# Kernel optimization log

Hardware: AMD Instinct MI355X
Metric: run time of the kernel (lower is better)

Reference implementation:

```python
import jax, jax.numpy as jnp
import numpy as np
from jax import lax

# Fixed dims from MSSMamba defaults
B_, L_, DM = 2, 8192, 256
NH, HP, NS = 4, 64, 8          # nheads, headdim, d_state
DIN = NH * HP                  # d_inner = 256
DPROJ = 2 * DIN + 2 * NS + NH  # 532


def setup_inputs() -> dict:
    key = jax.random.key(0)
    ks = jax.random.split(key, 16)
    f = lambda k, s, sc=1.0: jax.random.normal(k, s, jnp.float32) * sc
    inp = {
        'x_H': f(ks[0], (B_, L_, DM)),
        'x_V': f(ks[1], (B_, L_, DM)),
        'W_in_H': f(ks[2], (DM, 2 * DPROJ), 0.05),
        'W_in_V': f(ks[3], (DM, 2 * DPROJ), 0.05),
        'W_out_HF': f(ks[4], (DIN, DM), 0.05),
        'W_out_HB': f(ks[5], (DIN, DM), 0.05),
        'W_out_VF': f(ks[6], (DIN, DM), 0.05),
        'W_out_VB': f(ks[7], (DIN, DM), 0.05),
        'W_out': f(ks[8], (4 * DM, DM), 0.05),
    }
    for i, nm in enumerate(['HF', 'HB', 'VF', 'VB']):
        kd = jax.random.fold_in(ks[9], i)
        ka = jax.random.fold_in(ks[10], i)
        inp['dt_bias_' + nm] = f(kd, (NH,), 0.1)
        inp['A_log_' + nm] = jnp.log(jax.random.uniform(ka, (NH,), jnp.float32, 1.0, 16.0))
        inp['D_' + nm] = jnp.ones((NH,), jnp.float32)
    # per-batch permutation mapping vertical position -> horizontal position
    inp['v2h'] = jax.vmap(lambda k: jax.random.permutation(k, L_))(
        jax.random.split(ks[11], B_)).astype(jnp.int32)
    return inp


def _scan_dir(zxbcdt, dt_bias, A_log, D):
    # zxbcdt: [b, l, DPROJ] -> Mamba2-style selective scan, ngroups=1
    z = zxbcdt[..., :DIN].reshape(B_, L_, NH, HP)
    xBC = jax.nn.silu(zxbcdt[..., DIN:DIN + DIN + 2 * NS])
    x = xBC[..., :DIN].reshape(B_, L_, NH, HP)
    Bm = xBC[..., DIN:DIN + NS]      # [b, l, n]
    Cm = xBC[..., DIN + NS:]         # [b, l, n]
    dt = jax.nn.softplus(zxbcdt[..., -NH:] + dt_bias)  # [b, l, h]
    A = -jnp.exp(A_log)              # [h]
    dA = jnp.exp(dt * A)             # [b, l, h]
    dBx = jnp.einsum('blh,bln,blhp->blhpn', dt, Bm, x)  # [b,l,h,p,n]

    def step(state, inp):
        dA_t, dBx_t, C_t = inp
        state = dA_t[..., None, None] * state + dBx_t   # [b,h,p,n]
        y_t = jnp.einsum('bhpn,bn->bhp', state, C_t)
        return state, y_t

    init = jnp.zeros((B_, NH, HP, NS), dt.dtype)
    _, ys = lax.scan(step, init, (jnp.moveaxis(dA, 1, 0),
                                  jnp.moveaxis(dBx, 1, 0),
                                  jnp.moveaxis(Cm, 1, 0)))
    y = jnp.moveaxis(ys, 0, 1) + D[None, None, :, None] * x  # skip D*x
    y = y * jax.nn.silu(z)                                   # gate
    return y.reshape(B_, L_, DIN)


def reference(x_H, x_V, W_in_H, W_in_V,
              dt_bias_HF, dt_bias_HB, dt_bias_VF, dt_bias_VB,
              A_log_HF, A_log_HB, A_log_VF, A_log_VB,
              D_HF, D_HB, D_VF, D_VB,
              W_out_HF, W_out_HB, W_out_VF, W_out_VB,
              W_out, v2h):
    zx_HF, zx_HB = jnp.split(x_H @ W_in_H, 2, axis=-1)
    zx_VF, zx_VB = jnp.split(x_V @ W_in_V, 2, axis=-1)
    # note: source applies out_proj_HB to the HF branch (kept faithful)
    y_HF = _scan_dir(zx_HF, dt_bias_HF, A_log_HF, D_HF) @ W_out_HB
    y_HB = _scan_dir(zx_HB[:, ::-1], dt_bias_HB, A_log_HB, D_HB)[:, ::-1] @ W_out_HF
    y_VF = _scan_dir(zx_VF, dt_bias_VF, A_log_VF, D_VF) @ W_out_VB
    y_VB = _scan_dir(zx_VB[:, ::-1], dt_bias_VB, A_log_VB, D_VB)[:, ::-1] @ W_out_VF
    # remap vertical-ordered outputs to horizontal ordering (scatter by v2h)
    bidx = jnp.arange(B_)[:, None]
    y_VF = jnp.zeros_like(y_VF).at[bidx, v2h].set(y_VF)
    y_VB = jnp.zeros_like(y_VB).at[bidx, v2h].set(y_VB)
    cat = jnp.concatenate([y_HF, y_HB, y_VF, y_VB], axis=-1)  # [b, l, 4*d_model]
    return jax.nn.silu(cat) @ W_out
```

## Files before the change

### kernel.cpp

```cpp
#include <hip/hip_runtime.h>
#include <hip/hip_bf16.h>

#define B_N 2
#define L_N 8192
#define ROWS 16384
#define CHUNK 32
#define NCHUNK 256
#define NPAD 1152

typedef __bf16 bf16x8 __attribute__((ext_vector_type(8)));
typedef float f32x4 __attribute__((ext_vector_type(4)));

__device__ __forceinline__ float siluf(float v) {
  return v * __builtin_amdgcn_rcpf(1.f + __expf(-v));
}
__device__ __forceinline__ float softplusf_(float v) {
  return fmaxf(v, 0.f) + log1pf(__expf(-fabsf(v)));
}
__device__ __forceinline__ unsigned short f2bf(float v) {
  union { __bf16 b; unsigned short u; } x;
  x.b = (__bf16)v;
  return x.u;
}
__device__ __forceinline__ float bf2f(unsigned short u) {
  union { unsigned u; float f; } x; x.u = ((unsigned)u) << 16;
  return x.f;
}

__device__ __forceinline__ void gload_lds16(const unsigned short* g, unsigned short* l) {
  __builtin_amdgcn_global_load_lds(
      (const __attribute__((address_space(1))) unsigned int*)g,
      (__attribute__((address_space(3))) unsigned int*)l, 16, 0, 0);
}

struct P4 { const float* p[4]; };
struct ScanConsts {
  const float* dt_bias[4];
  const float* A_log[4];
  const float* D[4];
};

__global__ __launch_bounds__(256) void k_prep(
    const float* __restrict__ xH, const float* __restrict__ xV,
    const float* __restrict__ WH, const float* __restrict__ WV,
    P4 ws, const float* __restrict__ W_out, ScanConsts sc,
    unsigned short* __restrict__ xbf, float* __restrict__ dtv_arr, float* __restrict__ dA_arr,
    unsigned short* __restrict__ Wt_in, unsigned short* __restrict__ Wt_dirs,
    unsigned short* __restrict__ Wt_fin) {
  __shared__ float xs[32][257];
  __shared__ float Wsm[8][260];
  int bid = blockIdx.x;
  int tid = threadIdx.x;
  if (bid < 1024) {
    const int mat = bid >> 9;
    const float* x = mat ? xV : xH;
    const float* W = mat ? WV : WH;
    const int r0 = (bid & 511) * 32;
    for (int i = tid; i < 2048; i += 256) {
      int c = i >> 8, k = i & 255;
      int sl = c >> 2, h = c & 3;
      Wsm[c][k] = W[(long)k * 1064 + sl * 532 + 528 + h];
    }
    for (int i = tid; i < 32 * 64; i += 256) {
      int rl = i >> 6, kq = (i & 63) * 4;
      float4 v = *(const float4*)(x + (long)(r0 + rl) * 256 + kq);
      xs[rl][kq + 0] = v.x; xs[rl][kq + 1] = v.y; xs[rl][kq + 2] = v.z; xs[rl][kq + 3] = v.w;
    }
    __syncthreads();
    for (int i = tid; i < 32 * 64; i += 256) {
      int rl = i >> 6, kq = (i & 63) * 4;
      ushort4 o;
      o.x = f2bf(xs[rl][kq + 0]);
      o.y = f2bf(xs[rl][kq + 1]);
      o.z = f2bf(xs[rl][kq + 2]);
      o.w = f2bf(xs[rl][kq + 3]);
      *(ushort4*)(xbf + (size_t)mat * ROWS * 256 + (long)(r0 + rl) * 256 + kq) = o;
    }
    const int rl = tid >> 3, c = tid & 7;
    float s = 0.f;
    #pragma unroll 8
    for (int k = 0; k < 256; ++k) s = fmaf(xs[rl][k], Wsm[c][k], s);
    const int sl = c >> 2, h = c & 3;
    const int dir = mat * 2 + sl;
    float dtv = softplusf_(s + sc.dt_bias[dir][h]);
    float dAv = __expf(dtv * (-__expf(sc.A_log[dir][h])));
    long o = ((long)dir * 4 + h) * ROWS + (r0 + rl);
    dtv_arr[o] = dtv;
    dA_arr[o] = dAv;
  } else if (bid < 3328) {
    int i = (bid - 1024) * 256 + tid;
    int z = i / (NPAD * 256);
    int rem = i - z * (NPAD * 256);
    int n = rem >> 8, k = rem & 255;
    const float* W = z ? WV : WH;
    int sl = n >= 544;
    int cc = n - (sl ? 544 : 0);
    float v = (cc < 532) ? W[(long)k * 1064 + sl * 532 + cc] : 0.f;
    Wt_in[i] = f2bf(v);
  } else if (bid < 4352) {
    int i = (bid - 3328) * 256 + tid;
    int d = i >> 16;
    int rem = i & 65535;
    int n = rem >> 8, k = rem & 255;
    Wt_dirs[i] = f2bf(ws.p[d][(long)k * 256 + n]);
  } else {
    int i = (bid - 4352) * 256 + tid;
    int n = i >> 10, k = i & 1023;
    Wt_fin[i] = f2bf(W_out[(long)k * 256 + n]);
  }
}

struct EpiIn {
  unsigned short* zraw;
  unsigned short* xraw;
  unsigned short* bc;
};

__global__ __launch_bounds__(256) void k_gemm_in(
    const unsigned short* __restrict__ Abase, const unsigned short* __restrict__ Btbase,
    EpiIn ep) {
  __shared__ unsigned short As[128 * 32];
  __shared__ unsigned short Bs[128 * 32];
  __shared__ unsigned short trs[4][16 * 72];
  const int tid = threadIdx.x;
  const int lane = tid & 63;
  const int wid = tid >> 6;
  const int wm = wid & 1, wn = wid >> 1;
  const int q = lane >> 4, r = lane & 15;
  const int m0 = blockIdx.x * 128;
  const int n0 = blockIdx.y * 128;
  const int z = blockIdx.z;
  const unsigned short* A = Abase + (long)z * ROWS * 256;
  const unsigned short* Bt = Btbase + (long)z * NPAD * 256;

  f32x4 acc[4][4] = {};
  const int swr = (r >> 1) & 3;

  for (int kt = 0; kt < 256; kt += 32) {
    #pragma unroll
    for (int i = 0; i < 2; ++i) {
      int idx = i * 256 + tid;
      int row = idx >> 2;
      int ch = (idx & 3) ^ ((row >> 1) & 3);
      gload_lds16(A + (long)(m0 + row) * 256 + kt + ch * 8,
                  &As[(size_t)(i * 256 + wid * 64) * 8]);
    }
    #pragma unroll
    for (int i = 0; i < 2; ++i) {
      int idx = i * 256 + tid;
      int row = idx >> 2;
      int ch = (idx & 3) ^ ((row >> 1) & 3);
      gload_lds16(Bt + (long)(n0 + row) * 256 + kt + ch * 8,
                  &Bs[(size_t)(i * 256 + wid * 64) * 8]);
    }
    __syncthreads();
    bf16x8 af[4], bfr[4];
    #pragma unroll
    for (int mi = 0; mi < 4; ++mi)
      af[mi] = *(const bf16x8*)&As[((wm * 64 + mi * 16 + r) * 4 + (q ^ swr)) * 8];
    #pragma unroll
    for (int ni = 0; ni < 4; ++ni)
      bfr[ni] = *(const bf16x8*)&Bs[((wn * 64 + ni * 16 + r) * 4 + (q ^ swr)) * 8];
    #pragma unroll
    for (int mi = 0; mi < 4; ++mi)
      #pragma unroll
      for (int ni = 0; ni < 4; ++ni)
        acc[mi][ni] = __builtin_amdgcn_mfma_f32_16x16x32_bf16(af[mi], bfr[ni], acc[mi][ni], 0, 0, 0);
    __syncthreads();
  }

  unsigned short* tr = trs[wid];
  #pragma unroll
  for (int mi = 0; mi < 4; ++mi) {
    #pragma unroll
    for (int ni = 0; ni < 4; ++ni)
      #pragma unroll
      for (int j = 0; j < 4; ++j)
        tr[(q * 4 + j) * 72 + ni * 16 + r] = f2bf(acc[mi][ni][j]);
    asm volatile("s_waitcnt lgkmcnt(0)" ::: "memory");
    #pragma unroll
    for (int pass = 0; pass < 2; ++pass) {
      int rl = pass * 8 + (lane >> 3);
      int c8 = (lane & 7) * 8;
      bf16x8 v = *(const bf16x8*)&tr[rl * 72 + c8];
      int row = m0 + wm * 64 + mi * 16 + rl;
      int col = n0 + wn * 64 + c8;
      int sl = col >= 544;
      int cc = col - (sl ? 544 : 0);
      if (cc < 528) {
        int dir = z * 2 + sl;
        if (cc < 256)
          *(bf16x8*)(ep.zraw + ((long)dir * ROWS + row) * 256 + cc) = v;
        else if (cc < 512)
          *(bf16x8*)(ep.xraw + ((long)dir * ROWS + row) * 256 + cc - 256) = v;
        else
          *(bf16x8*)(ep.bc + ((long)dir * ROWS + row) * 16 + cc - 512) = v;
      }
    }
    asm volatile("s_waitcnt lgkmcnt(0)" ::: "memory");
  }
}

__global__ __launch_bounds__(512, 4) void k_fuse(
    const unsigned short* __restrict__ ybf,
    const unsigned short* __restrict__ Wt_dirs,
    const unsigned short* __restrict__ Wt_fin,
    unsigned short* __restrict__ pbuf) {
  __shared__ unsigned short Ab[2][64 * 32];
  __shared__ unsigned short Bb[2][256 * 32];
  __shared__ unsigned short Tl[64 * 264];
  const int tid = threadIdx.x;
  const int lane = tid & 63;
  const int wid = tid >> 6;
  const int wm = wid & 1, wn = wid >> 1;
  const int q = lane >> 4, r = lane & 15;
  const int r0 = blockIdx.x * 64;
  const int pair = blockIdx.y;
  const int swr = (r >> 1) & 3;

  const int a_row = tid >> 2;
  const int a_ch = (tid & 3) ^ ((a_row >> 1) & 3);
  const long a_off = (long)(r0 + a_row) * 256 + a_ch * 8;
  int b_row[2], b_ch[2];
  #pragma unroll
  for (int rnd = 0; rnd < 2; ++rnd) {
    int idx = rnd * 512 + tid;
    b_row[rnd] = idx >> 2;
    b_ch[rnd] = (idx & 3) ^ ((b_row[rnd] >> 1) & 3);
  }

  f32x4 acc_o[2][4] = {};
  int cur = 0;

  {
    const unsigned short* yd = ybf + (long)(pair * 2) * ROWS * 256;
    const unsigned short* Wd = Wt_dirs + (long)(pair * 2) * 65536;
    if (tid < 256)
      gload_lds16(yd + a_off, &Ab[0][(size_t)(wid * 64) * 8]);
    #pragma unroll
    for (int rnd = 0; rnd < 2; ++rnd)
      gload_lds16(Wd + (long)b_row[rnd] * 256 + b_ch[rnd] * 8,
                  &Bb[0][(size_t)(rnd * 512 + wid * 64) * 8]);
  }
  __syncthreads();

  #pragma unroll
  for (int dd = 0; dd < 2; ++dd) {
    const int d = pair * 2 + dd;
    const unsigned short* yd = ybf + (long)d * ROWS * 256;
    const unsigned short* Wd = Wt_dirs + (long)d * 65536;

    f32x4 acc_t[2][4] = {};
    for (int kt8 = 0; kt8 < 8; ++kt8) {
      const int kt = kt8 * 32;
      if (kt8 < 7) {
        if (tid < 256)
          gload_lds16(yd + a_off + kt + 32, &Ab[cur ^ 1][(size_t)(wid * 64) * 8]);
        #pragma unroll
        for (int rnd = 0; rnd < 2; ++rnd)
          gload_lds16(Wd + (long)b_row[rnd] * 256 + kt + 32 + b_ch[rnd] * 8,
                      &Bb[cur ^ 1][(size_t)(rnd * 512 + wid * 64) * 8]);
      } else {
        #pragma unroll
        for (int rnd = 0; rnd < 2; ++rnd)
          gload_lds16(Wt_fin + (long)b_row[rnd] * 1024 + d * 256 + b_ch[rnd] * 8,
                      &Bb[cur ^ 1][(size_t)(rnd * 512 + wid * 64) * 8]);
      }
      bf16x8 af[2], bfr[4];
      #pragma unroll
      for (int mi = 0; mi < 2; ++mi)
        af[mi] = *(const bf16x8*)&Ab[cur][((wm * 32 + mi * 16 + r) * 4 + (q ^ swr)) * 8];
      #pragma unroll
      for (int ni = 0; ni < 4; ++ni)
        bfr[ni] = *(const bf16x8*)&Bb[cur][((wn * 64 + ni * 16 + r) * 4 + (q ^ swr)) * 8];
      __builtin_amdgcn_s_setprio(1);
      #pragma unroll
      for (int mi = 0; mi < 2; ++mi)
        #pragma unroll
        for (int ni = 0; ni < 4; ++ni)
          acc_t[mi][ni] = __builtin_amdgcn_mfma_f32_16x16x32_bf16(af[mi], bfr[ni], acc_t[mi][ni], 0, 0, 0);
      __builtin_amdgcn_s_setprio(0);
      __syncthreads();
      cur ^= 1;
    }
    #pragma unroll
    for (int mi = 0; mi < 2; ++mi)
      #pragma unroll
      for (int ni = 0; ni < 4; ++ni)
        #pragma unroll
        for (int j = 0; j < 4; ++j)
          Tl[(wm * 32 + mi * 16 + q * 4 + j) * 264 + wn * 64 + ni * 16 + r] =
              f2bf(siluf(acc_t[mi][ni][j]));
    __syncthreads();
    for (int kt8 = 0; kt8 < 8; ++kt8) {
      const int kt = kt8 * 32;
      if (kt8 < 7) {
        #pragma unroll
        for (int rnd = 0; rnd < 2; ++rnd)
          gload_lds16(Wt_fin + (long)b_row[rnd] * 1024 + d * 256 + kt + 32 + b_ch[rnd] * 8,
                      &Bb[cur ^ 1][(size_t)(rnd * 512 + wid * 64) * 8]);
      } else if (dd == 0) {
        const unsigned short* yd1 = ybf + (long)(d + 1) * ROWS * 256;
        const unsigned short* Wd1 = Wt_dirs + (long)(d + 1) * 65536;
        if (tid < 256)
          gload_lds16(yd1 + a_off, &Ab[cur ^ 1][(size_t)(wid * 64) * 8]);
        #pragma unroll
        for (int rnd = 0; rnd < 2; ++rnd)
          gload_lds16(Wd1 + (long)b_row[rnd] * 256 + b_ch[rnd] * 8,
                      &Bb[cur ^ 1][(size_t)(rnd * 512 + wid * 64) * 8]);
      }
      bf16x8 af[2], bfr[4];
      #pragma unroll
      for (int mi = 0; mi < 2; ++mi)
        af[mi] = *(const bf16x8*)&Tl[(wm * 32 + mi * 16 + r) * 264 + kt + q * 8];
      #pragma unroll
      for (int ni = 0; ni < 4; ++ni)
        bfr[ni] = *(const bf16x8*)&Bb[cur][((wn * 64 + ni * 16 + r) * 4 + (q ^ swr)) * 8];
      __builtin_amdgcn_s_setprio(1);
      #pragma unroll
      for (int mi = 0; mi < 2; ++mi)
        #pragma unroll
        for (int ni = 0; ni < 4; ++ni)
          acc_o[mi][ni] = __builtin_amdgcn_mfma_f32_16x16x32_bf16(af[mi], bfr[ni], acc_o[mi][ni], 0, 0, 0);
      __builtin_amdgcn_s_setprio(0);
      __syncthreads();
      cur ^= 1;
    }
  }

  #pragma unroll
  for (int mi = 0; mi < 2; ++mi)
    #pragma unroll
    for (int ni = 0; ni < 4; ++ni)
      #pragma unroll
      for (int j = 0; j < 4; ++j)
        Tl[(wm * 32 + mi * 16 + q * 4 + j) * 264 + wn * 64 + ni * 16 + r] = f2bf(acc_o[mi][ni][j]);
  __syncthreads();
  unsigned short* pout = pbuf + (long)pair * ROWS * 256;
  #pragma unroll
  for (int pass = 0; pass < 4; ++pass) {
    int id = pass * 512 + tid;
    int row = id >> 5, c8 = (id & 31) * 8;
    bf16x8 v = *(const bf16x8*)&Tl[row * 264 + c8];
    *(bf16x8*)(pout + (long)(r0 + row) * 256 + c8) = v;
  }
}

__global__ void k_red(const unsigned short* __restrict__ pbuf, float* __restrict__ out) {
  int i = blockIdx.x * 256 + threadIdx.x;
  uint4 a = ((const uint4*)pbuf)[i];
  uint4 b = ((const uint4*)(pbuf + (size_t)ROWS * 256))[i];
  const unsigned short* au = (const unsigned short*)&a;
  const unsigned short* bu = (const unsigned short*)&b;
  float rr[8];
  #pragma unroll
  for (int j = 0; j < 8; ++j) rr[j] = bf2f(au[j]) + bf2f(bu[j]);
  ((float4*)out)[i * 2] = *(float4*)&rr[0];
  ((float4*)out)[i * 2 + 1] = *(float4*)&rr[4];
}

struct ScanP {
  const unsigned short* xraw;
  const unsigned short* zraw;
  const unsigned short* bc;
  const float* dtv;
  const float* dA;
  const float* D[4];
};

__global__ __launch_bounds__(64) void k_scan1(ScanP sp, float* __restrict__ S,
                                              float* __restrict__ P) {
  __shared__ __align__(16) float Bst[CHUNK][8];
  __shared__ float dAs[CHUNK];
  const int p = threadIdx.x;
  const int c = blockIdx.x;
  const int bh = blockIdx.y;
  const int d = blockIdx.z;
  const int b = bh >> 2, h = bh & 3;
  const int rev = d & 1;
  const int t0 = c * CHUNK;
  if (p < CHUNK) {
    const int t = t0 + p;
    const int l = rev ? (L_N - 1 - t) : t;
    const int row = (b << 13) + l;
    uint4 bv = *(const uint4*)(sp.bc + ((long)d * ROWS + row) * 16);
    const unsigned short* bu = (const unsigned short*)&bv;
    float dtvv = sp.dtv[((long)d * 4 + h) * ROWS + row];
    dAs[p] = sp.dA[((long)d * 4 + h) * ROWS + row];
    #pragma unroll
    for (int n = 0; n < 8; ++n) Bst[p][n] = siluf(bf2f(bu[n])) * dtvv;
  }
  __syncthreads();

  float st[8] = {0, 0, 0, 0, 0, 0, 0, 0};
  float cumdA = 1.f;
  const int l0 = rev ? (L_N - 1 - t0) : t0;
  const unsigned short* xp = sp.xraw + ((long)d * ROWS + (b << 13) + l0) * 256 + h * 64 + p;
  const long stp = rev ? -256L : 256L;

  unsigned short xa[8], xb[8];
  #pragma unroll
  for (int j = 0; j < 8; ++j) xa[j] = xp[(long)j * stp];
  #pragma unroll
  for (int g = 0; g < 4; ++g) {
    if (g < 3) {
      #pragma unroll
      for (int j = 0; j < 8; ++j) xb[j] = xp[(long)((g + 1) * 8 + j) * stp];
    }
    #pragma unroll
    for (int j = 0; j < 8; ++j) {
      int s = g * 8 + j;
      float x = siluf(bf2f(xa[j]));
      float dA = dAs[s];
      f32x4 B0 = *(const f32x4*)&Bst[s][0];
      f32x4 B1 = *(const f32x4*)&Bst[s][4];
      cumdA *= dA;
      st[0] = fmaf(dA, st[0], x * B0[0]);
      st[1] = fmaf(dA, st[1], x * B0[1]);
      st[2] = fmaf(dA, st[2], x * B0[2]);
      st[3] = fmaf(dA, st[3], x * B0[3]);
      st[4] = fmaf(dA, st[4], x * B1[0]);
      st[5] = fmaf(dA, st[5], x * B1[1]);
      st[6] = fmaf(dA, st[6], x * B1[2]);
      st[7] = fmaf(dA, st[7], x * B1[3]);
    }
    #pragma unroll
    for (int j = 0; j < 8; ++j) xa[j] = xb[j];
  }
  float* Sp = S + ((((long)d * NCHUNK + c) * 8 + bh) * 64 + p) * 8;
  #pragma unroll
  for (int n = 0; n < 8; ++n) Sp[n] = st[n];
  if (p == 0) P[((long)d * NCHUNK + c) * 8 + bh] = cumdA;
}

__global__ __launch_bounds__(512) void k_scan2(const float* __restrict__ S,
                                               const float* __restrict__ P,
                                               float* __restrict__ carry) {
  __shared__ float Pl[NCHUNK];
  const int tid = threadIdx.x;
  const int dbh = blockIdx.x;
  const int d = dbh >> 3, bh = dbh & 7;
  if (tid < NCHUNK) Pl[tid] = P[((long)d * NCHUNK + tid) * 8 + bh];
  __syncthreads();
  float cy = 0.f;
  carry[(((long)d * NCHUNK + 0) * 8 + bh) * 512 + tid] = 0.f;
  #pragma unroll 8
  for (int c = 1; c < NCHUNK; ++c) {
    const float Sv = S[(((long)d * NCHUNK + (c - 1)) * 8 + bh) * 512 + tid];
    cy = fmaf(Pl[c - 1], cy, Sv);
    carry[(((long)d * NCHUNK + c) * 8 + bh) * 512 + tid] = cy;
  }
}

__global__ __launch_bounds__(64) void k_scan3(ScanP sp, const float* __restrict__ carry,
                                              const int* __restrict__ v2h,
                                              unsigned short* __restrict__ ybf) {
  __shared__ __align__(16) float Bst[CHUNK][8];
  __shared__ __align__(16) float Cst[CHUNK][8];
  __shared__ float dAs[CHUNK];
  __shared__ int orow[CHUNK];
  const int p = threadIdx.x;
  const int c = blockIdx.x;
  const int bh = blockIdx.y;
  const int d = blockIdx.z;
  const int b = bh >> 2, h = bh & 3;
  const int rev = d & 1;
  const float Dv = sp.D[d][h];
  const int t0 = c * CHUNK;
  if (p < CHUNK) {
    const int t = t0 + p;
    const int l = rev ? (L_N - 1 - t) : t;
    const int row = (b << 13) + l;
    orow[p] = (d >= 2) ? v2h[b * L_N + l] : l;
    const unsigned short* bp = sp.bc + ((long)d * ROWS + row) * 16;
    uint4 bv = *(const uint4*)bp;
    uint4 cv = *(const uint4*)(bp + 8);
    const unsigned short* bu = (const unsigned short*)&bv;
    const unsigned short* cu = (const unsigned short*)&cv;
    float dtvv = sp.dtv[((long)d * 4 + h) * ROWS + row];
    dAs[p] = sp.dA[((long)d * 4 + h) * ROWS + row];
    #pragma unroll
    for (int n = 0; n < 8; ++n) Bst[p][n] = siluf(bf2f(bu[n])) * dtvv;
    #pragma unroll
    for (int n = 0; n < 8; ++n) Cst[p][n] = siluf(bf2f(cu[n]));
  }
  __syncthreads();

  float st[8];
  {
    const float* cp = carry + ((((long)d * NCHUNK + c) * 8 + bh) * 64 + p) * 8;
    #pragma unroll
    for (int n = 0; n < 8; ++n) st[n] = cp[n];
  }

  const int l0 = rev ? (L_N - 1 - t0) : t0;
  const long base = (long)(b << 13) + l0;
  const unsigned short* xp = sp.xraw + ((long)d * ROWS + base) * 256 + h * 64 + p;
  const unsigned short* zp = sp.zraw + ((long)d * ROWS + base) * 256 + h * 64 + p;
  unsigned short* yb = ybf + (long)d * ROWS * 256 + ((long)(b << 13)) * 256 + h * 64 + p;
  const long stp = rev ? -256L : 256L;

  unsigned short xa[8], xb[8], za[8], zb[8];
  #pragma unroll
  for (int j = 0; j < 8; ++j) { xa[j] = xp[(long)j * stp]; za[j] = zp[(long)j * stp]; }
  #pragma unroll
  for (int g = 0; g < 4; ++g) {
    if (g < 3) {
      #pragma unroll
      for (int j = 0; j < 8; ++j) {
        xb[j] = xp[(long)((g + 1) * 8 + j) * stp];
        zb[j] = zp[(long)((g + 1) * 8 + j) * stp];
      }
    }
    #pragma unroll
    for (int j = 0; j < 8; ++j) {
      int s = g * 8 + j;
      float x = siluf(bf2f(xa[j]));
      float zv = siluf(bf2f(za[j]));
      float dA = dAs[s];
      f32x4 B0 = *(const f32x4*)&Bst[s][0];
      f32x4 B1 = *(const f32x4*)&Bst[s][4];
      f32x4 C0 = *(const f32x4*)&Cst[s][0];
      f32x4 C1 = *(const f32x4*)&Cst[s][4];
      st[0] = fmaf(dA, st[0], x * B0[0]);
      st[1] = fmaf(dA, st[1], x * B0[1]);
      st[2] = fmaf(dA, st[2], x * B0[2]);
      st[3] = fmaf(dA, st[3], x * B0[3]);
      st[4] = fmaf(dA, st[4], x * B1[0]);
      st[5] = fmaf(dA, st[5], x * B1[1]);
      st[6] = fmaf(dA, st[6], x * B1[2]);
      st[7] = fmaf(dA, st[7], x * B1[3]);
      float y01 = fmaf(st[1], C0[1], st[0] * C0[0]);
      float y23 = fmaf(st[3], C0[3], st[2] * C0[2]);
      float y45 = fmaf(st[5], C1[1], st[4] * C1[0]);
      float y67 = fmaf(st[7], C1[3], st[6] * C1[2]);
      float y = (y01 + y23) + (y45 + y67);
      y = fmaf(Dv, x, y) * zv;
      yb[(long)orow[s] * 256] = f2bf(y);
    }
    #pragma unroll
    for (int j = 0; j < 8; ++j) { xa[j] = xb[j]; za[j] = zb[j]; }
  }
}

extern "C" void kernel_launch(void* const* d_in, const int* in_sizes, int n_in,
                              void* d_out, int out_size, void* d_ws, size_t ws_size,
                              hipStream_t stream) {
  const float* x_H = (const float*)d_in[0];
  const float* x_V = (const float*)d_in[1];
  const float* W_in_H = (const float*)d_in[2];
  const float* W_in_V = (const float*)d_in[3];
  const float* W_out_HF = (const float*)d_in[4];
  const float* W_out_HB = (const float*)d_in[5];
  const float* W_out_VF = (const float*)d_in[6];
  const float* W_out_VB = (const float*)d_in[7];
  const float* W_out = (const float*)d_in[8];
  const float* dt_bias_HF = (const float*)d_in[9];
  const float* A_log_HF = (const float*)d_in[10];
  const float* D_HF = (const float*)d_in[11];
  const float* dt_bias_HB = (const float*)d_in[12];
  const float* A_log_HB = (const float*)d_in[13];
  const float* D_HB = (const float*)d_in[14];
  const float* dt_bias_VF = (const float*)d_in[15];
  const float* A_log_VF = (const float*)d_in[16];
  const float* D_VF = (const float*)d_in[17];
  const float* dt_bias_VB = (const float*)d_in[18];
  const float* A_log_VB = (const float*)d_in[19];
  const float* D_VB = (const float*)d_in[20];
  const int* v2h = (const int*)d_in[21];

  char* ws = (char*)d_ws;
  size_t off = 0;
  auto alloc = [&](size_t bytes) {
    void* pp = ws + off;
    off = (off + bytes + 255) & ~(size_t)255;
    return pp;
  };
  unsigned short* xbf = (unsigned short*)alloc((size_t)2 * ROWS * 256 * 2);
  unsigned short* Wt_in = (unsigned short*)alloc((size_t)2 * NPAD * 256 * 2);
  unsigned short* Wt_dirs = (unsigned short*)alloc((size_t)4 * 65536 * 2);
  unsigned short* Wt_fin = (unsigned short*)alloc((size_t)256 * 1024 * 2);
  unsigned short* zraw = (unsigned short*)alloc((size_t)4 * ROWS * 256 * 2);
  unsigned short* xraw = (unsigned short*)alloc((size_t)4 * ROWS * 256 * 2);
  unsigned short* bc = (unsigned short*)alloc((size_t)4 * ROWS * 16 * 2);
  float* dtv_arr = (float*)alloc((size_t)16 * ROWS * 4);
  float* dA_arr = (float*)alloc((size_t)16 * ROWS * 4);
  unsigned short* ybf = (unsigned short*)alloc((size_t)4 * ROWS * 256 * 2);
  float* S = (float*)alloc((size_t)4 * NCHUNK * 8 * 512 * 4);
  float* P = (float*)alloc((size_t)4 * NCHUNK * 8 * 4);
  float* carry = (float*)alloc((size_t)4 * NCHUNK * 8 * 512 * 4);
  unsigned short* pbuf = (unsigned short*)alloc((size_t)2 * ROWS * 256 * 2);

  ScanConsts sc;
  sc.dt_bias[0] = dt_bias_HF; sc.dt_bias[1] = dt_bias_HB;
  sc.dt_bias[2] = dt_bias_VF; sc.dt_bias[3] = dt_bias_VB;
  sc.A_log[0] = A_log_HF; sc.A_log[1] = A_log_HB;
  sc.A_log[2] = A_log_VF; sc.A_log[3] = A_log_VB;
  sc.D[0] = D_HF; sc.D[1] = D_HB; sc.D[2] = D_VF; sc.D[3] = D_VB;

  P4 wdirs;
  wdirs.p[0] = W_out_HB; wdirs.p[1] = W_out_HF; wdirs.p[2] = W_out_VB; wdirs.p[3] = W_out_VF;

  k_prep<<<5376, 256, 0, stream>>>(x_H, x_V, W_in_H, W_in_V, wdirs, W_out, sc,
                                   xbf, dtv_arr, dA_arr, Wt_in, Wt_dirs, Wt_fin);

  EpiIn ep; ep.zraw = zraw; ep.xraw = xraw; ep.bc = bc;

  k_gemm_in<<<dim3(ROWS / 128, NPAD / 128, 2), 256, 0, stream>>>(xbf, Wt_in, ep);

  ScanP sp;
  sp.xraw = xraw; sp.zraw = zraw; sp.bc = bc; sp.dtv = dtv_arr; sp.dA = dA_arr;
  sp.D[0] = D_HF; sp.D[1] = D_HB; sp.D[2] = D_VF; sp.D[3] = D_VB;

  k_scan1<<<dim3(NCHUNK, 8, 4), 64, 0, stream>>>(sp, S, P);
  k_scan2<<<32, 512, 0, stream>>>(S, P, carry);
  k_scan3<<<dim3(NCHUNK, 8, 4), 64, 0, stream>>>(sp, carry, v2h, ybf);

  k_fuse<<<dim3(ROWS / 64, 2), 512, 0, stream>>>(ybf, Wt_dirs, Wt_fin, pbuf);
  k_red<<<ROWS * 256 / 8 / 256, 256, 0, stream>>>(pbuf, (float*)d_out);

  (void)in_sizes; (void)n_in; (void)out_size; (void)ws_size;
}
```

Measured before the change: 271.0 us.

## Double-buffer input GEMM, split carry scan hierarchically, move v2h scatter into reduction

The input GEMM now double-buffers its A/B LDS tiles, prefetching the next K slice while MFMAs run on the current one, and raises wave priority around the MFMAs. The serial 256-step carry scan is split into a two-level scan: 16 parallel groups of 16 chunks, then 16 group carries, with the prefix recombined in scan3. The scan output now stores contiguously instead of scattering rows through v2h. An inverse permutation built in k_prep lets the final reduction gather the vertical pair's rows instead. This shortens the serial dependency and removes scattered stores, at the cost of extra kernels, extra buffers and a gather in the reduction.

```diff
diff --git a/kernel.cpp b/kernel.cpp
--- a/kernel.cpp
+++ b/kernel.cpp
@@ -6,6 +6,8 @@
 #define ROWS 16384
 #define CHUNK 32
 #define NCHUNK 256
+#define GRP 16
+#define NGRP 16
 #define NPAD 1152
 
 typedef __bf16 bf16x8 __attribute__((ext_vector_type(8)));
@@ -43,10 +45,10 @@
 __global__ __launch_bounds__(256) void k_prep(
     const float* __restrict__ xH, const float* __restrict__ xV,
     const float* __restrict__ WH, const float* __restrict__ WV,
-    P4 ws, const float* __restrict__ W_out, ScanConsts sc,
+    P4 ws, const float* __restrict__ W_out, const int* __restrict__ v2h, ScanConsts sc,
     unsigned short* __restrict__ xbf, float* __restrict__ dtv_arr, float* __restrict__ dA_arr,
     unsigned short* __restrict__ Wt_in, unsigned short* __restrict__ Wt_dirs,
-    unsigned short* __restrict__ Wt_fin) {
+    unsigned short* __restrict__ Wt_fin, int* __restrict__ inv) {
   __shared__ float xs[32][257];
   __shared__ float Wsm[8][260];
   int bid = blockIdx.x;
@@ -103,10 +105,16 @@
     int rem = i & 65535;
     int n = rem >> 8, k = rem & 255;
     Wt_dirs[i] = f2bf(ws.p[d][(long)k * 256 + n]);
-  } else {
+  } else if (bid < 5376) {
     int i = (bid - 4352) * 256 + tid;
     int n = i >> 10, k = i & 1023;
     Wt_fin[i] = f2bf(W_out[(long)k * 256 + n]);
+  } else {
+    int m = (bid - 5376) * 256 + tid;
+    if (m < ROWS) {
+      int b = m >> 13;
+      inv[b * L_N + v2h[m]] = m;
+    }
   }
 }
 
@@ -119,9 +127,9 @@
 __global__ __launch_bounds__(256) void k_gemm_in(
     const unsigned short* __restrict__ Abase, const unsigned short* __restrict__ Btbase,
     EpiIn ep) {
-  __shared__ unsigned short As[128 * 32];
-  __shared__ unsigned short Bs[128 * 32];
-  __shared__ unsigned short trs[4][16 * 72];
+  __shared__ unsigned short smem[16384];
+  unsigned short* AsB = smem;
+  unsigned short* BsB = smem + 8192;
   const int tid = threadIdx.x;
   const int lane = tid & 63;
   const int wid = tid >> 6;
@@ -133,43 +141,57 @@
   const unsigned short* A = Abase + (long)z * ROWS * 256;
   const unsigned short* Bt = Btbase + (long)z * NPAD * 256;
 
+  int s_row[2], s_ch[2];
+  #pragma unroll
+  for (int i = 0; i < 2; ++i) {
+    int idx = i * 256 + tid;
+    s_row[i] = idx >> 2;
+    s_ch[i] = (idx & 3) ^ ((s_row[i] >> 1) & 3);
+  }
+
   f32x4 acc[4][4] = {};
   const int swr = (r >> 1) & 3;
-
-  for (int kt = 0; kt < 256; kt += 32) {
-    #pragma unroll
-    for (int i = 0; i < 2; ++i) {
-      int idx = i * 256 + tid;
-      int row = idx >> 2;
-      int ch = (idx & 3) ^ ((row >> 1) & 3);
-      gload_lds16(A + (long)(m0 + row) * 256 + kt + ch * 8,
-                  &As[(size_t)(i * 256 + wid * 64) * 8]);
-    }
-    #pragma unroll
-    for (int i = 0; i < 2; ++i) {
-      int idx = i * 256 + tid;
-      int row = idx >> 2;
-      int ch = (idx & 3) ^ ((row >> 1) & 3);
-      gload_lds16(Bt + (long)(n0 + row) * 256 + kt + ch * 8,
-                  &Bs[(size_t)(i * 256 + wid * 64) * 8]);
-    }
-    __syncthreads();
+  int cur = 0;
+
+  #pragma unroll
+  for (int i = 0; i < 2; ++i) {
+    gload_lds16(A + (long)(m0 + s_row[i]) * 256 + s_ch[i] * 8,
+                AsB + (size_t)(i * 256 + wid * 64) * 8);
+    gload_lds16(Bt + (long)(n0 + s_row[i]) * 256 + s_ch[i] * 8,
+                BsB + (size_t)(i * 256 + wid * 64) * 8);
+  }
+  __syncthreads();
+
+  for (int kt8 = 0; kt8 < 8; ++kt8) {
+    const int kt = kt8 * 32;
+    if (kt8 < 7) {
+      #pragma unroll
+      for (int i = 0; i < 2; ++i) {
+        gload_lds16(A + (long)(m0 + s_row[i]) * 256 + kt + 32 + s_ch[i] * 8,
+                    AsB + (size_t)((cur ^ 1) * 4096 + (i * 256 + wid * 64) * 8));
+        gload_lds16(Bt + (long)(n0 + s_row[i]) * 256 + kt + 32 + s_ch[i] * 8,
+                    BsB + (size_t)((cur ^ 1) * 4096 + (i * 256 + wid * 64) * 8));
+      }
+    }
     bf16x8 af[4], bfr[4];
     #pragma unroll
     for (int mi = 0; mi < 4; ++mi)
-      af[mi] = *(const bf16x8*)&As[((wm * 64 + mi * 16 + r) * 4 + (q ^ swr)) * 8];
+      af[mi] = *(const bf16x8*)&AsB[cur * 4096 + ((wm * 64 + mi * 16 + r) * 4 + (q ^ swr)) * 8];
     #pragma unroll
     for (int ni = 0; ni < 4; ++ni)
-      bfr[ni] = *(const bf16x8*)&Bs[((wn * 64 + ni * 16 + r) * 4 + (q ^ swr)) * 8];
+      bfr[ni] = *(const bf16x8*)&BsB[cur * 4096 + ((wn * 64 + ni * 16 + r) * 4 + (q ^ swr)) * 8];
+    __builtin_amdgcn_s_setprio(1);
     #pragma unroll
     for (int mi = 0; mi < 4; ++mi)
       #pragma unroll
       for (int ni = 0; ni < 4; ++ni)
         acc[mi][ni] = __builtin_amdgcn_mfma_f32_16x16x32_bf16(af[mi], bfr[ni], acc[mi][ni], 0, 0, 0);
+    __builtin_amdgcn_s_setprio(0);
     __syncthreads();
-  }
-
-  unsigned short* tr = trs[wid];
+    cur ^= 1;
+  }
+
+  unsigned short* tr = smem + wid * (16 * 72);
   #pragma unroll
   for (int mi = 0; mi < 4; ++mi) {
     #pragma unroll
@@ -346,10 +368,13 @@
   }
 }
 
-__global__ void k_red(const unsigned short* __restrict__ pbuf, float* __restrict__ out) {
+__global__ void k_red(const unsigned short* __restrict__ pbuf,
+                      const int* __restrict__ inv, float* __restrict__ out) {
   int i = blockIdx.x * 256 + threadIdx.x;
-  uint4 a = ((const uint4*)pbuf)[i];
-  uint4 b = ((const uint4*)(pbuf + (size_t)ROWS * 256))[i];
+  int row = i >> 5, c8 = (i & 31) * 8;
+  uint4 a = *(const uint4*)(pbuf + (long)row * 256 + c8);
+  int vrow = inv[row];
+  uint4 b = *(const uint4*)(pbuf + (size_t)ROWS * 256 + (long)vrow * 256 + c8);
   const unsigned short* au = (const unsigned short*)&a;
   const unsigned short* bu = (const unsigned short*)&b;
   float rr[8];
@@ -433,32 +458,63 @@
   if (p == 0) P[((long)d * NCHUNK + c) * 8 + bh] = cumdA;
 }
 
-__global__ __launch_bounds__(512) void k_scan2(const float* __restrict__ S,
-                                               const float* __restrict__ P,
-                                               float* __restrict__ carry) {
-  __shared__ float Pl[NCHUNK];
+__global__ __launch_bounds__(512) void k_scan2a(const float* __restrict__ S,
+                                                const float* __restrict__ P,
+                                                float* __restrict__ carry_loc,
+                                                float* __restrict__ Sg,
+                                                float* __restrict__ Pg) {
+  __shared__ float Pl[GRP];
+  const int tid = threadIdx.x;
+  const int gid = blockIdx.x;
+  const int g = gid & 15;
+  const int dbh = gid >> 4;
+  const int d = dbh >> 3, bh = dbh & 7;
+  if (tid < GRP) Pl[tid] = P[((long)d * NCHUNK + g * GRP + tid) * 8 + bh];
+  __syncthreads();
+  float cy = 0.f;
+  #pragma unroll
+  for (int i = 0; i < GRP; ++i) {
+    const int c = g * GRP + i;
+    carry_loc[(((long)d * NCHUNK + c) * 8 + bh) * 512 + tid] = cy;
+    const float Sv = S[(((long)d * NCHUNK + c) * 8 + bh) * 512 + tid];
+    cy = fmaf(Pl[i], cy, Sv);
+  }
+  Sg[(((long)d * NGRP + g) * 8 + bh) * 512 + tid] = cy;
+  if (tid == 0) {
+    float pp = 1.f;
+    #pragma unroll
+    for (int i = 0; i < GRP; ++i) pp *= Pl[i];
+    Pg[((long)d * NGRP + g) * 8 + bh] = pp;
+  }
+}
+
+__global__ __launch_bounds__(512) void k_scan2b(const float* __restrict__ Sg,
+                                                const float* __restrict__ Pg,
+                                                float* __restrict__ gcarry) {
+  __shared__ float Pgl[NGRP];
   const int tid = threadIdx.x;
   const int dbh = blockIdx.x;
   const int d = dbh >> 3, bh = dbh & 7;
-  if (tid < NCHUNK) Pl[tid] = P[((long)d * NCHUNK + tid) * 8 + bh];
+  if (tid < NGRP) Pgl[tid] = Pg[((long)d * NGRP + tid) * 8 + bh];
   __syncthreads();
   float cy = 0.f;
-  carry[(((long)d * NCHUNK + 0) * 8 + bh) * 512 + tid] = 0.f;
-  #pragma unroll 8
-  for (int c = 1; c < NCHUNK; ++c) {
-    const float Sv = S[(((long)d * NCHUNK + (c - 1)) * 8 + bh) * 512 + tid];
-    cy = fmaf(Pl[c - 1], cy, Sv);
-    carry[(((long)d * NCHUNK + c) * 8 + bh) * 512 + tid] = cy;
-  }
-}
-
-__global__ __launch_bounds__(64) void k_scan3(ScanP sp, const float* __restrict__ carry,
-                                              const int* __restrict__ v2h,
+  #pragma unroll
+  for (int g = 0; g < NGRP; ++g) {
+    gcarry[(((long)d * NGRP + g) * 8 + bh) * 512 + tid] = cy;
+    const float Sv = Sg[(((long)d * NGRP + g) * 8 + bh) * 512 + tid];
+    cy = fmaf(Pgl[g], cy, Sv);
+  }
+}
+
+__global__ __launch_bounds__(64) void k_scan3(ScanP sp,
+                                              const float* __restrict__ carry_loc,
+                                              const float* __restrict__ gcarry,
+                                              const float* __restrict__ Pc,
                                               unsigned short* __restrict__ ybf) {
   __shared__ __align__(16) float Bst[CHUNK][8];
   __shared__ __align__(16) float Cst[CHUNK][8];
   __shared__ float dAs[CHUNK];
-  __shared__ int orow[CHUNK];
+  __shared__ float Pgr[GRP];
   const int p = threadIdx.x;
   const int c = blockIdx.x;
   const int bh = blockIdx.y;
@@ -467,11 +523,12 @@
   const int rev = d & 1;
   const float Dv = sp.D[d][h];
   const int t0 = c * CHUNK;
+  const int grp = c >> 4, ii = c & 15;
+  if (p < ii) Pgr[p] = Pc[((long)d * NCHUNK + grp * GRP + p) * 8 + bh];
   if (p < CHUNK) {
     const int t = t0 + p;
     const int l = rev ? (L_N - 1 - t) : t;
     const int row = (b << 13) + l;
-    orow[p] = (d >= 2) ? v2h[b * L_N + l] : l;
     const unsigned short* bp = sp.bc + ((long)d * ROWS + row) * 16;
     uint4 bv = *(const uint4*)bp;
     uint4 cv = *(const uint4*)(bp + 8);
@@ -486,18 +543,21 @@
   }
   __syncthreads();
 
+  float pref = 1.f;
+  for (int k = 0; k < ii; ++k) pref *= Pgr[k];
   float st[8];
   {
-    const float* cp = carry + ((((long)d * NCHUNK + c) * 8 + bh) * 64 + p) * 8;
-    #pragma unroll
-    for (int n = 0; n < 8; ++n) st[n] = cp[n];
+    const float* clp = carry_loc + ((((long)d * NCHUNK + c) * 8 + bh) * 64 + p) * 8;
+    const float* gcp = gcarry + ((((long)d * NGRP + grp) * 8 + bh) * 64 + p) * 8;
+    #pragma unroll
+    for (int n = 0; n < 8; ++n) st[n] = fmaf(pref, gcp[n], clp[n]);
   }
 
   const int l0 = rev ? (L_N - 1 - t0) : t0;
   const long base = (long)(b << 13) + l0;
   const unsigned short* xp = sp.xraw + ((long)d * ROWS + base) * 256 + h * 64 + p;
   const unsigned short* zp = sp.zraw + ((long)d * ROWS + base) * 256 + h * 64 + p;
-  unsigned short* yb = ybf + (long)d * ROWS * 256 + ((long)(b << 13)) * 256 + h * 64 + p;
+  unsigned short* yp = ybf + ((long)d * ROWS + base) * 256 + h * 64 + p;
   const long stp = rev ? -256L : 256L;
 
   unsigned short xa[8], xb[8], za[8], zb[8];
@@ -536,7 +596,7 @@
       float y67 = fmaf(st[7], C1[3], st[6] * C1[2]);
       float y = (y01 + y23) + (y45 + y67);
       y = fmaf(Dv, x, y) * zv;
-      yb[(long)orow[s] * 256] = f2bf(y);
+      yp[(long)s * stp] = f2bf(y);
     }
     #pragma unroll
     for (int j = 0; j < 8; ++j) { xa[j] = xb[j]; za[j] = zb[j]; }
@@ -588,7 +648,11 @@
   unsigned short* ybf = (unsigned short*)alloc((size_t)4 * ROWS * 256 * 2);
   float* S = (float*)alloc((size_t)4 * NCHUNK * 8 * 512 * 4);
   float* P = (float*)alloc((size_t)4 * NCHUNK * 8 * 4);
-  float* carry = (float*)alloc((size_t)4 * NCHUNK * 8 * 512 * 4);
+  float* carry_loc = (float*)alloc((size_t)4 * NCHUNK * 8 * 512 * 4);
+  float* Sg = (float*)alloc((size_t)4 * NGRP * 8 * 512 * 4);
+  float* Pg = (float*)alloc((size_t)4 * NGRP * 8 * 4);
+  float* gcarry = (float*)alloc((size_t)4 * NGRP * 8 * 512 * 4);
+  int* inv = (int*)alloc((size_t)ROWS * 4);
   unsigned short* pbuf = (unsigned short*)alloc((size_t)2 * ROWS * 256 * 2);
 
   ScanConsts sc;
@@ -601,8 +665,8 @@
   P4 wdirs;
   wdirs.p[0] = W_out_HB; wdirs.p[1] = W_out_HF; wdirs.p[2] = W_out_VB; wdirs.p[3] = W_out_VF;
 
-  k_prep<<<5376, 256, 0, stream>>>(x_H, x_V, W_in_H, W_in_V, wdirs, W_out, sc,
-                                   xbf, dtv_arr, dA_arr, Wt_in, Wt_dirs, Wt_fin);
+  k_prep<<<5440, 256, 0, stream>>>(x_H, x_V, W_in_H, W_in_V, wdirs, W_out, v2h, sc,
+                                   xbf, dtv_arr, dA_arr, Wt_in, Wt_dirs, Wt_fin, inv);
 
   EpiIn ep; ep.zraw = zraw; ep.xraw = xraw; ep.bc = bc;
 
@@ -613,11 +677,12 @@
   sp.D[0] = D_HF; sp.D[1] = D_HB; sp.D[2] = D_VF; sp.D[3] = D_VB;
 
   k_scan1<<<dim3(NCHUNK, 8, 4), 64, 0, stream>>>(sp, S, P);
-  k_scan2<<<32, 512, 0, stream>>>(S, P, carry);
-  k_scan3<<<dim3(NCHUNK, 8, 4), 64, 0, stream>>>(sp, carry, v2h, ybf);
+  k_scan2a<<<512, 512, 0, stream>>>(S, P, carry_loc, Sg, Pg);
+  k_scan2b<<<32, 512, 0, stream>>>(Sg, Pg, gcarry);
+  k_scan3<<<dim3(NCHUNK, 8, 4), 64, 0, stream>>>(sp, carry_loc, gcarry, P, ybf);
 
   k_fuse<<<dim3(ROWS / 64, 2), 512, 0, stream>>>(ybf, Wt_dirs, Wt_fin, pbuf);
-  k_red<<<ROWS * 256 / 8 / 256, 256, 0, stream>>>(pbuf, (float*)d_out);
+  k_red<<<ROWS * 256 / 8 / 256, 256, 0, stream>>>(pbuf, inv, (float*)d_out);
 
   (void)in_sizes; (void)n_in; (void)out_size; (void)ws_size;
 }
```

New measurement: 254.2 us. 1.07x faster.
